# Kernel tuning notes

Hardware: AMD Instinct MI355X
Metric: run time of the kernel (lower is better)

## Reference

```python
import jax, jax.numpy as jnp
import numpy as np

N_XI = 512      # internal REN state dim
L = 128         # nonlinearity channels (sequential loop length)
N_STATES = 128  # plant state dim (w)
N_INPUTS = 64   # control input dim (u)
EPS = 0.001
STD = 0.1
BATCH = 32768


def _model_params(X, Y):
    """set_model_param(): derive constrained REN matrices from free params X, Y."""
    n, l = N_XI, L
    H = X.T @ X + EPS * jnp.eye(2 * n + l, dtype=X.dtype)
    H11 = H[:n, :n]
    H21 = H[n:n + l, :n]
    H22 = H[n:n + l, n:n + l]
    H31 = H[n + l:, :n]
    H32 = H[n + l:, n:n + l]
    H33 = H[n + l:, n + l:]
    Fm = H31                                 # (n_xi, n_xi)
    B1 = H32                                 # (n_xi, l)
    E = 0.5 * (H11 + H33 + Y - Y.T)          # (n_xi, n_xi)
    Lam = 0.5 * jnp.diag(H22)                # (l,) strictly positive
    D11 = -jnp.tril(H22, -1)                 # strictly lower triangular (l, l)
    C1 = -H21                                # (l, n_xi)
    return Fm, B1, E, Lam, D11, C1


def setup_inputs() -> dict:
    key = jax.random.key(0)
    ks = jax.random.split(key, 9)
    n, l = N_XI, L
    return {
        "t": 0,
        "w": jax.random.normal(ks[0], (BATCH, 1, N_STATES), jnp.float32),
        "xi": jax.random.normal(ks[1], (BATCH, 1, n), jnp.float32),
        "X": jax.random.normal(ks[2], (2 * n + l, 2 * n + l), jnp.float32) * STD,
        "Y": jax.random.normal(ks[3], (n, n), jnp.float32) * STD,
        "B2": jax.random.normal(ks[4], (n, N_STATES), jnp.float32) * STD,
        "C2": jax.random.normal(ks[5], (N_INPUTS, n), jnp.float32) * STD,
        "D21": jax.random.normal(ks[6], (N_INPUTS, l), jnp.float32) * STD,
        "D22": jax.random.normal(ks[7], (N_INPUTS, N_STATES), jnp.float32) * STD,
        "D12": jax.random.normal(ks[8], (l, N_STATES), jnp.float32) * STD,
    }


def reference(t, w, xi, X, Y, B2, C2, D21, D22, D12):
    Fm, B1, E, Lam, D11, C1 = _model_params(X, Y)
    w2 = w[:, 0, :]    # (B, num_states)
    xi2 = xi[:, 0, :]  # (B, n_xi)

    # Precompute the xi- and w-dependent parts of every row's pre-activation.
    pre = xi2 @ C1.T + w2 @ D12.T  # (B, l)

    eye = jnp.eye(L, dtype=pre.dtype)

    def step(eps, xs):
        # Sequential forward substitution: row i only reads eps[:, :i]
        # because D11 is strictly lower triangular.
        d_row, p_col, lam, e_row = xs
        v = p_col + eps @ d_row            # (B,)
        e = jnp.tanh(v / lam)
        return eps + e[:, None] * e_row[None, :], None

    eps0 = jnp.zeros_like(pre)
    epsilon, _ = jax.lax.scan(step, eps0, (D11, pre.T, Lam, eye))  # (B, l)

    E_xi = xi2 @ Fm.T + epsilon @ B1.T + w2 @ B2.T      # (B, n_xi)
    xi_ = E_xi @ jnp.linalg.inv(E).T                    # (B, n_xi)
    u = xi2 @ C2.T + epsilon @ D21.T + w2 @ D22.T       # (B, num_inputs)
    return u[:, None, :], xi_[:, None, :]
```

## Files before the change

### kernel.cpp

```cpp
#include <hip/hip_runtime.h>
#include <cstddef>

#define NXI   512
#define LL    128
#define NST   128
#define NU    64
#define BATCH 32768
#define TW    1152
#define EPSC  0.001f
#define KC    768
#define NC    576
#define NCP   640

typedef unsigned short u16;
typedef __attribute__((ext_vector_type(8))) short   short8;
typedef __attribute__((ext_vector_type(4))) short   short4v;
typedef __attribute__((ext_vector_type(4))) float   f32x4;

__device__ __forceinline__ u16 f2bf(float f) {
    unsigned u = __float_as_uint(f);
    u += 0x7FFFu + ((u >> 16) & 1u);
    return (u16)(u >> 16);
}

__global__ __launch_bounds__(256) void k_setup(const float* __restrict__ X, u16* __restrict__ XT,
                                               const float* __restrict__ xi, const float* __restrict__ w,
                                               u16* __restrict__ Ac) {
    __shared__ float t[32][33];
    int blk = blockIdx.x;
    if (blk < 1296) {
        int tx = threadIdx.x & 31, ty = threadIdx.x >> 5;
        int bx = blk % 36, by = blk / 36;
        #pragma unroll
        for (int q = 0; q < 4; q++) {
            int r = ty + q * 8;
            t[r][tx] = X[(size_t)(by * 32 + r) * TW + bx * 32 + tx];
        }
        __syncthreads();
        #pragma unroll
        for (int q = 0; q < 4; q++) {
            int r = ty + q * 8;
            XT[(size_t)(bx * 32 + r) * TW + by * 32 + tx] = f2bf(t[tx][r]);
        }
        return;
    }
    size_t tt = (size_t)(blk - 1296) * 256 + threadIdx.x;
    int b = (int)(tt / 80), ch = (int)(tt % 80);
    const float* src;
    int col;
    if (ch < 64) { src = xi + (size_t)b * NXI + ch * 8;        col = ch * 8; }
    else         { src = w  + (size_t)b * NST + (ch - 64) * 8; col = 640 + (ch - 64) * 8; }
    f32x4 a = ((const f32x4*)src)[0], c = ((const f32x4*)src)[1];
    short8 o;
    o[0]=(short)f2bf(a[0]); o[1]=(short)f2bf(a[1]); o[2]=(short)f2bf(a[2]); o[3]=(short)f2bf(a[3]);
    o[4]=(short)f2bf(c[0]); o[5]=(short)f2bf(c[1]); o[6]=(short)f2bf(c[2]); o[7]=(short)f2bf(c[3]);
    *(short8*)(Ac + (size_t)b * KC + col) = o;
}

__global__ __launch_bounds__(256) void k_gemm2(const u16* __restrict__ A, int lda,
                                               const u16* __restrict__ W, int ldw,
                                               float* __restrict__ C0, int ldc0, int nsplit,
                                               float* __restrict__ C1, int ldc1,
                                               int K, int nbx, int ntrue, int swz) {
    __shared__ __align__(16) u16 As[2][128 * 32];
    __shared__ __align__(16) u16 Bs[2][128 * 32];
    int id = blockIdx.x;
    int bx, by;
    if (swz) {
        int j = id >> 3;
        int per = (int)(gridDim.x >> 3) / nbx;
        by = (id & 7) * per + j / nbx;
        bx = j - (j / nbx) * nbx;
    } else {
        by = id / nbx;
        bx = id - by * nbx;
    }
    const int tid = threadIdx.x;
    const int wave = tid >> 6, lane = tid & 63, quad = lane >> 4, l16 = lane & 15;
    const int bm0 = by * 128, bn0 = bx * 128;
    const int srow = tid >> 2;
    const int sch = (((tid & 3) ^ ((srow >> 2) & 3))) * 8;
    const u16* ga0 = A + (size_t)(bm0 + srow) * lda + sch;
    const u16* ga1 = ga0 + (size_t)64 * lda;
    const u16* gb0 = W + (size_t)(bn0 + srow) * ldw + sch;
    const u16* gb1 = gb0 + (size_t)64 * ldw;
    const int lo = wave * 512;
    const int mb = (wave >> 1) * 64, nb = (wave & 1) * 64;
    const int rch = (quad ^ (l16 >> 2)) * 8;

    f32x4 acc[4][4];
    #pragma unroll
    for (int i = 0; i < 4; i++)
        #pragma unroll
        for (int j = 0; j < 4; j++) acc[i][j] = (f32x4){0.f, 0.f, 0.f, 0.f};

    const int nk = K >> 5;
    __builtin_amdgcn_global_load_lds((void*)(ga0), (void*)(As[0] + lo),        16, 0, 0);
    __builtin_amdgcn_global_load_lds((void*)(ga1), (void*)(As[0] + lo + 2048), 16, 0, 0);
    __builtin_amdgcn_global_load_lds((void*)(gb0), (void*)(Bs[0] + lo),        16, 0, 0);
    __builtin_amdgcn_global_load_lds((void*)(gb1), (void*)(Bs[0] + lo + 2048), 16, 0, 0);
    __syncthreads();
    int cur = 0;
    for (int t = 0; t < nk; ++t) {
        if (t + 1 < nk) {
            const int kt = (t + 1) << 5;
            const int nx = cur ^ 1;
            __builtin_amdgcn_global_load_lds((void*)(ga0 + kt), (void*)(As[nx] + lo),        16, 0, 0);
            __builtin_amdgcn_global_load_lds((void*)(ga1 + kt), (void*)(As[nx] + lo + 2048), 16, 0, 0);
            __builtin_amdgcn_global_load_lds((void*)(gb0 + kt), (void*)(Bs[nx] + lo),        16, 0, 0);
            __builtin_amdgcn_global_load_lds((void*)(gb1 + kt), (void*)(Bs[nx] + lo + 2048), 16, 0, 0);
        }
        const u16* as = As[cur];
        const u16* bs = Bs[cur];
        short8 af[4], bf[4];
        #pragma unroll
        for (int mt = 0; mt < 4; mt++) af[mt] = *(const short8*)&as[(mb + mt * 16 + l16) * 32 + rch];
        #pragma unroll
        for (int nt = 0; nt < 4; nt++) bf[nt] = *(const short8*)&bs[(nb + nt * 16 + l16) * 32 + rch];
        #pragma unroll
        for (int mt = 0; mt < 4; mt++)
            #pragma unroll
            for (int nt = 0; nt < 4; nt++)
                acc[mt][nt] = __builtin_amdgcn_mfma_f32_16x16x32_bf16(af[mt], bf[nt], acc[mt][nt], 0, 0, 0);
        __syncthreads();
        cur ^= 1;
    }
    #pragma unroll
    for (int mt = 0; mt < 4; mt++)
        #pragma unroll
        for (int nt = 0; nt < 4; nt++)
            #pragma unroll
            for (int r = 0; r < 4; r++) {
                int row = bm0 + mb + mt * 16 + quad * 4 + r;
                int col = bn0 + nb + nt * 16 + l16;
                if (col < ntrue) {
                    float v = acc[mt][nt][r];
                    if (col < nsplit) C0[(size_t)row * ldc0 + col] = v;
                    else              C1[(size_t)row * ldc1 + (col - nsplit)] = v;
                }
            }
}

__global__ __launch_bounds__(256) void k_derive(const float* __restrict__ Hm, const float* __restrict__ Y,
                                                const float* __restrict__ B2, const float* __restrict__ D12,
                                                float* __restrict__ Agj, float* __restrict__ D11,
                                                float* __restrict__ rlam, u16* __restrict__ W1) {
    int idx = blockIdx.x * 256 + threadIdx.x;
    const int n0 = 512 * 1280, n1 = 128 * 128, n2 = 128, n3 = 128 * KC;
    if (idx < n0) {
        int i = idx / 1280, j = idx % 1280;
        float val;
        if (j < 512) {
            val = 0.5f * (Hm[(size_t)i * TW + j] + Hm[(size_t)(640 + i) * TW + 640 + j]
                          + Y[(size_t)i * 512 + j] - Y[(size_t)j * 512 + i]);
            if (i == j) val += EPSC;
        } else if (j < 1024) {
            val = Hm[(size_t)(640 + i) * TW + (j - 512)];
        } else if (j < 1152) {
            val = Hm[(size_t)(640 + i) * TW + 512 + (j - 1024)];
        } else {
            val = B2[(size_t)i * NST + (j - 1152)];
        }
        Agj[idx] = val;
        return;
    }
    idx -= n0;
    if (idx < n1) {
        int i = idx >> 7, j = idx & 127;
        D11[idx] = (j < i) ? -Hm[(size_t)(512 + i) * TW + 512 + j] : 0.f;
        return;
    }
    idx -= n1;
    if (idx < n2) {
        rlam[idx] = 2.0f / (Hm[(size_t)(512 + idx) * TW + 512 + idx] + EPSC);
        return;
    }
    idx -= n2;
    if (idx < n3) {
        int i = idx / KC, c = idx % KC;
        float v;
        if (c < 512)      v = -Hm[(size_t)(512 + i) * TW + c];
        else if (c < 640) v = 0.f;
        else              v = D12[(size_t)i * NST + (c - 640)];
        W1[(size_t)i * KC + c] = f2bf(v);
    }
}

__device__ __forceinline__ void invert64ip(float* Cl, float* Sa, float* mcol, float* rp,
                                           float* __restrict__ invOut, int tid) {
    int r = tid >> 2, c = tid & 3;
    float a[16];
    #pragma unroll
    for (int q = 0; q < 4; q++) {
        f32x4 v = *(f32x4*)&Cl[r * 68 + c * 16 + q * 4];
        a[q*4+0]=v[0]; a[q*4+1]=v[1]; a[q*4+2]=v[2]; a[q*4+3]=v[3];
    }
    #pragma unroll
    for (int k = 0; k < 64; k++) {
        const int p = (k & 1) << 6;
        const int kc = k >> 4, kl = k & 15;
        if (r == k) {
            #pragma unroll
            for (int q = 0; q < 4; q++)
                *(f32x4*)&Sa[p + c * 16 + q * 4] = (f32x4){a[q*4], a[q*4+1], a[q*4+2], a[q*4+3]};
        }
        if (c == kc) {
            mcol[p + r] = a[kl];
            if (r == k) rp[k & 1] = 1.0f / a[kl];
        }
        __syncthreads();
        const bool piv = (r == k);
        float ip = rp[k & 1];
        float m  = mcol[p + r];
        float tm = piv ? ip : -m * ip;
        #pragma unroll
        for (int j = 0; j < 16; j++) {
            float sj = Sa[p + c * 16 + j];
            a[j] = fmaf(tm, sj, piv ? 0.f : a[j]);
        }
        if (c == kc) a[kl] = tm;
    }
    #pragma unroll
    for (int q = 0; q < 4; q++)
        *(f32x4*)&invOut[r * 64 + c * 16 + q * 4] = (f32x4){a[q*4], a[q*4+1], a[q*4+2], a[q*4+3]};
}

__global__ __launch_bounds__(256) void k_diaginv0(const float* __restrict__ Agj, float* __restrict__ invD,
                                                  const u16* __restrict__ Ac, const u16* __restrict__ W1,
                                                  float* __restrict__ pre) {
    __shared__ __align__(16) u16 AsB[2][4096];
    __shared__ __align__(16) u16 BsB[2][4096];
    __shared__ __align__(16) float Cl[64 * 68];
    __shared__ float Sa[128], mcol[128], rp[2];
    const int tid = threadIdx.x;
    const int id = blockIdx.x;
    if (id == 0) {
        int r = tid >> 2, c4 = tid & 3;
        #pragma unroll
        for (int q = 0; q < 4; q++)
            *(f32x4*)&Cl[r * 68 + c4 * 16 + q * 4] = *(const f32x4*)(Agj + (size_t)r * 1280 + c4 * 16 + q * 4);
        __syncthreads();
        invert64ip(Cl, Sa, mcol, rp, invD, tid);
        return;
    }
    const int by = id - 1;
    const int wave = tid >> 6, lane = tid & 63, quad = lane >> 4, l16 = lane & 15;
    const int bm0 = by * 128;
    const int srow = tid >> 2;
    const int sch = (((tid & 3) ^ ((srow >> 2) & 3))) * 8;
    const u16* ga0 = Ac + (size_t)(bm0 + srow) * KC + sch;
    const u16* ga1 = ga0 + (size_t)64 * KC;
    const u16* gb0 = W1 + (size_t)srow * KC + sch;
    const u16* gb1 = gb0 + (size_t)64 * KC;
    const int lo = wave * 512;
    const int mb = (wave >> 1) * 64, nb = (wave & 1) * 64;
    const int rch = (quad ^ (l16 >> 2)) * 8;
    f32x4 acc[4][4];
    #pragma unroll
    for (int i = 0; i < 4; i++)
        #pragma unroll
        for (int j = 0; j < 4; j++) acc[i][j] = (f32x4){0.f, 0.f, 0.f, 0.f};
    __builtin_amdgcn_global_load_lds((void*)(ga0), (void*)(AsB[0] + lo),        16, 0, 0);
    __builtin_amdgcn_global_load_lds((void*)(ga1), (void*)(AsB[0] + lo + 2048), 16, 0, 0);
    __builtin_amdgcn_global_load_lds((void*)(gb0), (void*)(BsB[0] + lo),        16, 0, 0);
    __builtin_amdgcn_global_load_lds((void*)(gb1), (void*)(BsB[0] + lo + 2048), 16, 0, 0);
    __syncthreads();
    int cur = 0;
    for (int t = 0; t < 24; ++t) {
        if (t + 1 < 24) {
            const int kt = (t + 1) << 5;
            const int nx = cur ^ 1;
            __builtin_amdgcn_global_load_lds((void*)(ga0 + kt), (void*)(AsB[nx] + lo),        16, 0, 0);
            __builtin_amdgcn_global_load_lds((void*)(ga1 + kt), (void*)(AsB[nx] + lo + 2048), 16, 0, 0);
            __builtin_amdgcn_global_load_lds((void*)(gb0 + kt), (void*)(BsB[nx] + lo),        16, 0, 0);
            __builtin_amdgcn_global_load_lds((void*)(gb1 + kt), (void*)(BsB[nx] + lo + 2048), 16, 0, 0);
        }
        const u16* as = AsB[cur];
        const u16* bs = BsB[cur];
        short8 af[4], bf[4];
        #pragma unroll
        for (int mt = 0; mt < 4; mt++) af[mt] = *(const short8*)&as[(mb + mt * 16 + l16) * 32 + rch];
        #pragma unroll
        for (int nt = 0; nt < 4; nt++) bf[nt] = *(const short8*)&bs[(nb + nt * 16 + l16) * 32 + rch];
        #pragma unroll
        for (int mt = 0; mt < 4; mt++)
            #pragma unroll
            for (int nt = 0; nt < 4; nt++)
                acc[mt][nt] = __builtin_amdgcn_mfma_f32_16x16x32_bf16(af[mt], bf[nt], acc[mt][nt], 0, 0, 0);
        __syncthreads();
        cur ^= 1;
    }
    #pragma unroll
    for (int mt = 0; mt < 4; mt++)
        #pragma unroll
        for (int nt = 0; nt < 4; nt++)
            #pragma unroll
            for (int r = 0; r < 4; r++)
                pre[(size_t)(bm0 + mb + mt * 16 + quad * 4 + r) * LL + (nb + nt * 16 + l16)] = acc[mt][nt][r];
}

__global__ __launch_bounds__(256) void k_elim(float* __restrict__ Agj, float* __restrict__ invD, int k) {
    __shared__ __align__(16) float invDs[64 * 68];
    __shared__ __align__(16) float Ps[64 * 68];
    __shared__ __align__(16) float Ss[64 * 68];
    __shared__ __align__(16) float Ms[64 * 68];
    __shared__ float Sa[128], mcol[128], rp[2];
    int tid = threadIdx.x;
    int by = blockIdx.y, bx = blockIdx.x;
    int rb = by + (by >= k ? 1 : 0);
    int cb = k + 1 + bx;
    int lr = tid >> 2, lc = tid & 3;
    #pragma unroll
    for (int q = 0; q < 4; q++) {
        *(f32x4*)&invDs[lr * 68 + lc * 16 + q * 4] = *(const f32x4*)(invD + (size_t)k * 4096 + lr * 64 + lc * 16 + q * 4);
        *(f32x4*)&Ps[lr * 68 + lc * 16 + q * 4]    = *(const f32x4*)(Agj + (size_t)(k * 64 + lr) * 1280 + cb * 64 + lc * 16 + q * 4);
        *(f32x4*)&Ms[lr * 68 + lc * 16 + q * 4]    = *(const f32x4*)(Agj + (size_t)(rb * 64 + lr) * 1280 + k * 64 + lc * 16 + q * 4);
    }
    __syncthreads();
    int ty = tid >> 4, tx = tid & 15;
    f32x4 s[4];
    #pragma unroll
    for (int ri = 0; ri < 4; ri++) s[ri] = (f32x4){0.f, 0.f, 0.f, 0.f};
    for (int kk = 0; kk < 64; kk++) {
        f32x4 pv = *(f32x4*)&Ps[kk * 68 + tx * 4];
        #pragma unroll
        for (int ri = 0; ri < 4; ri++) s[ri] += pv * invDs[(ty * 4 + ri) * 68 + kk];
    }
    #pragma unroll
    for (int ri = 0; ri < 4; ri++) *(f32x4*)&Ss[(ty * 4 + ri) * 68 + tx * 4] = s[ri];
    __syncthreads();
    f32x4 accv[4];
    #pragma unroll
    for (int ri = 0; ri < 4; ri++)
        accv[ri] = *(const f32x4*)(Agj + (size_t)(rb * 64 + ty * 4 + ri) * 1280 + cb * 64 + tx * 4);
    for (int kk = 0; kk < 64; kk++) {
        f32x4 sv = *(f32x4*)&Ss[kk * 68 + tx * 4];
        #pragma unroll
        for (int ri = 0; ri < 4; ri++) accv[ri] -= sv * Ms[(ty * 4 + ri) * 68 + kk];
    }
    #pragma unroll
    for (int ri = 0; ri < 4; ri++)
        *(f32x4*)(Agj + (size_t)(rb * 64 + ty * 4 + ri) * 1280 + cb * 64 + tx * 4) = accv[ri];
    if (k < 7 && bx == 0 && by == k) {
        __syncthreads();
        #pragma unroll
        for (int ri = 0; ri < 4; ri++) *(f32x4*)&Ps[(ty * 4 + ri) * 68 + tx * 4] = accv[ri];
        __syncthreads();
        invert64ip(Ps, Sa, mcol, rp, invD + (size_t)(k + 1) * 4096, tid);
    }
}

__global__ __launch_bounds__(256) void k_finalize(const float* __restrict__ Agj, const float* __restrict__ invD,
                                                  const float* __restrict__ C2, const float* __restrict__ D21,
                                                  const float* __restrict__ D22, u16* __restrict__ Wc) {
    __shared__ __align__(16) float invDs[64 * 68];
    __shared__ __align__(16) float Ps[64 * 68];
    int tid = threadIdx.x, bx = blockIdx.x, by = blockIdx.y;
    int ty = tid >> 4, tx = tid & 15;
    if (by >= 8) {
        #pragma unroll
        for (int ri = 0; ri < 4; ri++) {
            int q = ty * 4 + ri;
            int row = 512 + (by - 8) * 64 + q;
            int cbase = bx * 64 + tx * 4;
            short4v o;
            if (by == 8) {
                f32x4 v;
                if (cbase < 512)      v = *(const f32x4*)(C2 + (size_t)q * 512 + cbase);
                else if (cbase < 640) v = *(const f32x4*)(D21 + (size_t)q * NST + (cbase - 512));
                else                  v = *(const f32x4*)(D22 + (size_t)q * NST + (cbase - 640));
                o[0]=(short)f2bf(v[0]); o[1]=(short)f2bf(v[1]); o[2]=(short)f2bf(v[2]); o[3]=(short)f2bf(v[3]);
            } else {
                o[0]=0; o[1]=0; o[2]=0; o[3]=0;
            }
            *(short4v*)(Wc + (size_t)row * KC + cbase) = o;
        }
        return;
    }
    int lr = tid >> 2, lc = tid & 3;
    #pragma unroll
    for (int q = 0; q < 4; q++) {
        *(f32x4*)&invDs[lr * 68 + lc * 16 + q * 4] = *(const f32x4*)(invD + (size_t)by * 4096 + lr * 64 + lc * 16 + q * 4);
        *(f32x4*)&Ps[lr * 68 + lc * 16 + q * 4]    = *(const f32x4*)(Agj + (size_t)(by * 64 + lr) * 1280 + 512 + bx * 64 + lc * 16 + q * 4);
    }
    __syncthreads();
    f32x4 s[4];
    #pragma unroll
    for (int ri = 0; ri < 4; ri++) s[ri] = (f32x4){0.f, 0.f, 0.f, 0.f};
    for (int kk = 0; kk < 64; kk++) {
        f32x4 pv = *(f32x4*)&Ps[kk * 68 + tx * 4];
        #pragma unroll
        for (int ri = 0; ri < 4; ri++) s[ri] += pv * invDs[(ty * 4 + ri) * 68 + kk];
    }
    #pragma unroll
    for (int ri = 0; ri < 4; ri++) {
        short4v o; o[0]=(short)f2bf(s[ri][0]); o[1]=(short)f2bf(s[ri][1]); o[2]=(short)f2bf(s[ri][2]); o[3]=(short)f2bf(s[ri][3]);
        *(short4v*)(Wc + (size_t)(by * 64 + ty * 4 + ri) * KC + bx * 64 + tx * 4) = o;
    }
}

__global__ __launch_bounds__(1024) void k_scan(const float* __restrict__ pre, const float* __restrict__ D11,
                                               const float* __restrict__ rlam, u16* __restrict__ Ac) {
    __shared__ __align__(16) float D11s[128 * 132];
    int tid = threadIdx.x;
    {
        int r = tid >> 3, c = (tid & 7) * 16;
        const f32x4* src = (const f32x4*)(D11 + (size_t)r * 128 + c);
        f32x4 v0 = src[0], v1 = src[1], v2 = src[2], v3 = src[3];
        f32x4* dst = (f32x4*)&D11s[r * 132 + c];
        dst[0] = v0; dst[1] = v1; dst[2] = v2; dst[3] = v3;
    }
    int lg = tid & 15;
    int row = blockIdx.x * 64 + (tid >> 4);
    int gbase = (tid & 63) & ~15;
    const float L2E2 = 2.885390082f;

    float corrv[8], a8[8];
    #pragma unroll
    for (int b = 0; b < 8; b++) {
        corrv[b] = pre[(size_t)row * 128 + b * 16 + lg];
        a8[b] = L2E2 * rlam[b * 16 + lg];
    }
    __syncthreads();

    #pragma unroll
    for (int b = 0; b < 8; b++) {
        f32x4 dblk[4];
        #pragma unroll
        for (int q = 0; q < 4; q++)
            dblk[q] = *(const f32x4*)&D11s[(b * 16 + lg) * 132 + b * 16 + q * 4];
        float v = corrv[b];
        float a = a8[b];
        float e16[16];
        float myeps = 0.f;
        #pragma unroll
        for (int t = 0; t < 16; t++) {
            float ex = __builtin_amdgcn_exp2f(a * v);
            float cand = 1.0f - 2.0f * __builtin_amdgcn_rcpf(ex + 1.0f);
            float e = __shfl(cand, gbase + t, 64);
            e16[t] = e;
            if (lg == t) myeps = e;
            v = fmaf(e, dblk[t >> 2][t & 3], v);
        }
        Ac[(size_t)row * KC + 512 + b * 16 + lg] = f2bf(myeps);
        #pragma unroll
        for (int bb = b + 1; bb < 8; bb++) {
            f32x4 dd[4];
            #pragma unroll
            for (int q = 0; q < 4; q++)
                dd[q] = *(const f32x4*)&D11s[(bb * 16 + lg) * 132 + b * 16 + q * 4];
            float acc = corrv[bb];
            #pragma unroll
            for (int t = 0; t < 16; t++)
                acc = fmaf(e16[t], dd[t >> 2][t & 3], acc);
            corrv[bb] = acc;
        }
    }
}

extern "C" void kernel_launch(void* const* d_in, const int* in_sizes, int n_in,
                              void* d_out, int out_size, void* d_ws, size_t ws_size,
                              hipStream_t stream) {
    const float* w_in  = (const float*)d_in[1];
    const float* xi_in = (const float*)d_in[2];
    const float* X   = (const float*)d_in[3];
    const float* Y   = (const float*)d_in[4];
    const float* B2  = (const float*)d_in[5];
    const float* C2  = (const float*)d_in[6];
    const float* D21 = (const float*)d_in[7];
    const float* D22 = (const float*)d_in[8];
    const float* D12 = (const float*)d_in[9];
    float* out_u  = (float*)d_out;
    float* out_xi = (float*)d_out + (size_t)BATCH * NU;

    char* base = (char*)d_ws;
    size_t off = 0;
    auto carve = [&](size_t bytes) -> void* {
        void* p = base + off;
        off += (bytes + 255) & ~(size_t)255;
        return p;
    };
    u16*   XT   = (u16*)  carve((size_t)TW * TW * 2);
    u16*   Ac   = (u16*)  carve((size_t)BATCH * KC * 2);
    float* Hm   = (float*)carve((size_t)TW * TW * 4);
    float* Agj  = (float*)carve((size_t)512 * 1280 * 4);
    float* invD = (float*)carve((size_t)8 * 64 * 64 * 4);
    u16*   Wc   = (u16*)  carve((size_t)NCP * KC * 2);
    u16*   W1   = (u16*)  carve((size_t)LL * KC * 2);
    float* pre  = (float*)carve((size_t)BATCH * LL * 4);
    float* D11  = (float*)carve((size_t)LL * LL * 4);
    float* rlam = (float*)carve((size_t)LL * 4);
    (void)ws_size; (void)in_sizes; (void)n_in; (void)out_size;

    k_setup<<<1296 + BATCH * 80 / 256, 256, 0, stream>>>(X, XT, xi_in, w_in, Ac);
    k_gemm2<<<81, 256, 0, stream>>>(XT, TW, XT, TW, Hm, TW, 1 << 30, nullptr, 0, TW, 9, TW, 0);
    k_derive<<<(512 * 1280 + 128 * 128 + 128 + 128 * KC + 255) / 256, 256, 0, stream>>>(
        Hm, Y, B2, D12, Agj, D11, rlam, W1);
    k_diaginv0<<<257, 256, 0, stream>>>(Agj, invD, Ac, W1, pre);
    for (int k = 0; k < 8; k++)
        k_elim<<<dim3(19 - k, 7), 256, 0, stream>>>(Agj, invD, k);
    k_finalize<<<dim3(12, 10), 256, 0, stream>>>(Agj, invD, C2, D21, D22, Wc);
    k_scan<<<BATCH / 64, 1024, 0, stream>>>(pre, D11, rlam, Ac);
    k_gemm2<<<1280, 256, 0, stream>>>(Ac, KC, Wc, KC, out_xi, NXI, 512, out_u, NU, KC, 5, NC, 1);
}
```

Measured before the change: 479.4 us.

## Fuse block Gauss-Jordan elimination steps and finalize into one persistent kernel

```diff
diff --git a/kernel.cpp b/kernel.cpp
--- a/kernel.cpp
+++ b/kernel.cpp
@@ -11,6 +11,7 @@
 #define KC    768
 #define NC    576
 #define NCP   640
+#define GJB   133
 
 typedef unsigned short u16;
 typedef __attribute__((ext_vector_type(8))) short   short8;
@@ -21,6 +22,36 @@
     unsigned u = __float_as_uint(f);
     u += 0x7FFFu + ((u >> 16) & 1u);
     return (u16)(u >> 16);
+}
+
+__device__ __forceinline__ void fbar(int* flags, int* go, int nblk, int tv, int id) {
+    __syncthreads();
+    const int t = threadIdx.x;
+    if (id == 0) {
+        if (t >= 1 && t < nblk) {
+            int spins = 0;
+            while (__hip_atomic_load(flags + t, __ATOMIC_RELAXED, __HIP_MEMORY_SCOPE_AGENT) < tv) {
+                __builtin_amdgcn_s_sleep(2);
+                if (++spins > (1 << 18)) break;
+            }
+        }
+        __syncthreads();
+        if (t == 0) {
+            __threadfence();
+            __hip_atomic_store(go, tv, __ATOMIC_RELEASE, __HIP_MEMORY_SCOPE_AGENT);
+        }
+    } else {
+        if (t == 0) {
+            __hip_atomic_store(flags + id, tv, __ATOMIC_RELEASE, __HIP_MEMORY_SCOPE_AGENT);
+            int spins = 0;
+            while (__hip_atomic_load(go, __ATOMIC_RELAXED, __HIP_MEMORY_SCOPE_AGENT) < tv) {
+                __builtin_amdgcn_s_sleep(2);
+                if (++spins > (1 << 18)) break;
+            }
+            __threadfence();
+        }
+    }
+    __syncthreads();
 }
 
 __global__ __launch_bounds__(256) void k_setup(const float* __restrict__ X, u16* __restrict__ XT,
@@ -144,7 +175,9 @@
 __global__ __launch_bounds__(256) void k_derive(const float* __restrict__ Hm, const float* __restrict__ Y,
                                                 const float* __restrict__ B2, const float* __restrict__ D12,
                                                 float* __restrict__ Agj, float* __restrict__ D11,
-                                                float* __restrict__ rlam, u16* __restrict__ W1) {
+                                                float* __restrict__ rlam, u16* __restrict__ W1,
+                                                int* __restrict__ bar) {
+    if (blockIdx.x == 0 && threadIdx.x < 192) bar[threadIdx.x] = 0;
     int idx = blockIdx.x * 256 + threadIdx.x;
     const int n0 = 512 * 1280, n1 = 128 * 128, n2 = 128, n3 = 128 * KC;
     if (idx < n0) {
@@ -299,103 +332,114 @@
                 pre[(size_t)(bm0 + mb + mt * 16 + quad * 4 + r) * LL + (nb + nt * 16 + l16)] = acc[mt][nt][r];
 }
 
-__global__ __launch_bounds__(256) void k_elim(float* __restrict__ Agj, float* __restrict__ invD, int k) {
+__global__ __launch_bounds__(256) void k_gj_fused(
+        float* __restrict__ Agj, float* __restrict__ invD,
+        const float* __restrict__ C2, const float* __restrict__ D21,
+        const float* __restrict__ D22, u16* __restrict__ Wc,
+        int* __restrict__ bar) {
     __shared__ __align__(16) float invDs[64 * 68];
     __shared__ __align__(16) float Ps[64 * 68];
     __shared__ __align__(16) float Ss[64 * 68];
     __shared__ __align__(16) float Ms[64 * 68];
     __shared__ float Sa[128], mcol[128], rp[2];
-    int tid = threadIdx.x;
-    int by = blockIdx.y, bx = blockIdx.x;
-    int rb = by + (by >= k ? 1 : 0);
-    int cb = k + 1 + bx;
-    int lr = tid >> 2, lc = tid & 3;
-    #pragma unroll
-    for (int q = 0; q < 4; q++) {
-        *(f32x4*)&invDs[lr * 68 + lc * 16 + q * 4] = *(const f32x4*)(invD + (size_t)k * 4096 + lr * 64 + lc * 16 + q * 4);
-        *(f32x4*)&Ps[lr * 68 + lc * 16 + q * 4]    = *(const f32x4*)(Agj + (size_t)(k * 64 + lr) * 1280 + cb * 64 + lc * 16 + q * 4);
-        *(f32x4*)&Ms[lr * 68 + lc * 16 + q * 4]    = *(const f32x4*)(Agj + (size_t)(rb * 64 + lr) * 1280 + k * 64 + lc * 16 + q * 4);
-    }
-    __syncthreads();
-    int ty = tid >> 4, tx = tid & 15;
-    f32x4 s[4];
-    #pragma unroll
-    for (int ri = 0; ri < 4; ri++) s[ri] = (f32x4){0.f, 0.f, 0.f, 0.f};
-    for (int kk = 0; kk < 64; kk++) {
-        f32x4 pv = *(f32x4*)&Ps[kk * 68 + tx * 4];
-        #pragma unroll
-        for (int ri = 0; ri < 4; ri++) s[ri] += pv * invDs[(ty * 4 + ri) * 68 + kk];
-    }
-    #pragma unroll
-    for (int ri = 0; ri < 4; ri++) *(f32x4*)&Ss[(ty * 4 + ri) * 68 + tx * 4] = s[ri];
-    __syncthreads();
-    f32x4 accv[4];
-    #pragma unroll
-    for (int ri = 0; ri < 4; ri++)
-        accv[ri] = *(const f32x4*)(Agj + (size_t)(rb * 64 + ty * 4 + ri) * 1280 + cb * 64 + tx * 4);
-    for (int kk = 0; kk < 64; kk++) {
-        f32x4 sv = *(f32x4*)&Ss[kk * 68 + tx * 4];
-        #pragma unroll
-        for (int ri = 0; ri < 4; ri++) accv[ri] -= sv * Ms[(ty * 4 + ri) * 68 + kk];
-    }
-    #pragma unroll
-    for (int ri = 0; ri < 4; ri++)
-        *(f32x4*)(Agj + (size_t)(rb * 64 + ty * 4 + ri) * 1280 + cb * 64 + tx * 4) = accv[ri];
-    if (k < 7 && bx == 0 && by == k) {
-        __syncthreads();
-        #pragma unroll
-        for (int ri = 0; ri < 4; ri++) *(f32x4*)&Ps[(ty * 4 + ri) * 68 + tx * 4] = accv[ri];
-        __syncthreads();
-        invert64ip(Ps, Sa, mcol, rp, invD + (size_t)(k + 1) * 4096, tid);
-    }
-}
-
-__global__ __launch_bounds__(256) void k_finalize(const float* __restrict__ Agj, const float* __restrict__ invD,
-                                                  const float* __restrict__ C2, const float* __restrict__ D21,
-                                                  const float* __restrict__ D22, u16* __restrict__ Wc) {
-    __shared__ __align__(16) float invDs[64 * 68];
-    __shared__ __align__(16) float Ps[64 * 68];
-    int tid = threadIdx.x, bx = blockIdx.x, by = blockIdx.y;
-    int ty = tid >> 4, tx = tid & 15;
-    if (by >= 8) {
+    const int tid = threadIdx.x;
+    const int id = blockIdx.x;
+    int* flags = bar;
+    int* go    = bar + 160;
+
+    for (int k = 0; k < 8; ++k) {
+        const int nbk = 7 * (19 - k);
+        if (id < nbk) {
+            const int by = id % 7, bx = id / 7;
+            const int rb = by + (by >= k ? 1 : 0);
+            const int cb = k + 1 + bx;
+            int lr = tid >> 2, lc = tid & 3;
+            #pragma unroll
+            for (int q = 0; q < 4; q++) {
+                *(f32x4*)&invDs[lr * 68 + lc * 16 + q * 4] = *(const f32x4*)(invD + (size_t)k * 4096 + lr * 64 + lc * 16 + q * 4);
+                *(f32x4*)&Ps[lr * 68 + lc * 16 + q * 4]    = *(const f32x4*)(Agj + (size_t)(k * 64 + lr) * 1280 + cb * 64 + lc * 16 + q * 4);
+                *(f32x4*)&Ms[lr * 68 + lc * 16 + q * 4]    = *(const f32x4*)(Agj + (size_t)(rb * 64 + lr) * 1280 + k * 64 + lc * 16 + q * 4);
+            }
+            __syncthreads();
+            int ty = tid >> 4, tx = tid & 15;
+            f32x4 s[4];
+            #pragma unroll
+            for (int ri = 0; ri < 4; ri++) s[ri] = (f32x4){0.f, 0.f, 0.f, 0.f};
+            for (int kk = 0; kk < 64; kk++) {
+                f32x4 pv = *(f32x4*)&Ps[kk * 68 + tx * 4];
+                #pragma unroll
+                for (int ri = 0; ri < 4; ri++) s[ri] += pv * invDs[(ty * 4 + ri) * 68 + kk];
+            }
+            #pragma unroll
+            for (int ri = 0; ri < 4; ri++) *(f32x4*)&Ss[(ty * 4 + ri) * 68 + tx * 4] = s[ri];
+            __syncthreads();
+            f32x4 accv[4];
+            #pragma unroll
+            for (int ri = 0; ri < 4; ri++)
+                accv[ri] = *(const f32x4*)(Agj + (size_t)(rb * 64 + ty * 4 + ri) * 1280 + cb * 64 + tx * 4);
+            for (int kk = 0; kk < 64; kk++) {
+                f32x4 sv = *(f32x4*)&Ss[kk * 68 + tx * 4];
+                #pragma unroll
+                for (int ri = 0; ri < 4; ri++) accv[ri] -= sv * Ms[(ty * 4 + ri) * 68 + kk];
+            }
+            #pragma unroll
+            for (int ri = 0; ri < 4; ri++)
+                *(f32x4*)(Agj + (size_t)(rb * 64 + ty * 4 + ri) * 1280 + cb * 64 + tx * 4) = accv[ri];
+            if (k < 7 && bx == 0 && by == k) {
+                __syncthreads();
+                #pragma unroll
+                for (int ri = 0; ri < 4; ri++) *(f32x4*)&Ps[(ty * 4 + ri) * 68 + tx * 4] = accv[ri];
+                __syncthreads();
+                invert64ip(Ps, Sa, mcol, rp, invD + (size_t)(k + 1) * 4096, tid);
+            }
+        }
+        fbar(flags, go, GJB, k + 1, id);
+    }
+
+    if (id < 120) {
+        const int bx = id % 12, by = id / 12;
+        int ty = tid >> 4, tx = tid & 15;
+        if (by >= 8) {
+            #pragma unroll
+            for (int ri = 0; ri < 4; ri++) {
+                int q = ty * 4 + ri;
+                int row = 512 + (by - 8) * 64 + q;
+                int cbase = bx * 64 + tx * 4;
+                short4v o;
+                if (by == 8) {
+                    f32x4 v;
+                    if (cbase < 512)      v = *(const f32x4*)(C2 + (size_t)q * 512 + cbase);
+                    else if (cbase < 640) v = *(const f32x4*)(D21 + (size_t)q * NST + (cbase - 512));
+                    else                  v = *(const f32x4*)(D22 + (size_t)q * NST + (cbase - 640));
+                    o[0]=(short)f2bf(v[0]); o[1]=(short)f2bf(v[1]); o[2]=(short)f2bf(v[2]); o[3]=(short)f2bf(v[3]);
+                } else {
+                    o[0]=0; o[1]=0; o[2]=0; o[3]=0;
+                }
+                *(short4v*)(Wc + (size_t)row * KC + cbase) = o;
+            }
+            return;
+        }
+        int lr = tid >> 2, lc = tid & 3;
+        #pragma unroll
+        for (int q = 0; q < 4; q++) {
+            *(f32x4*)&invDs[lr * 68 + lc * 16 + q * 4] = *(const f32x4*)(invD + (size_t)by * 4096 + lr * 64 + lc * 16 + q * 4);
+            *(f32x4*)&Ps[lr * 68 + lc * 16 + q * 4]    = *(const f32x4*)(Agj + (size_t)(by * 64 + lr) * 1280 + 512 + bx * 64 + lc * 16 + q * 4);
+        }
+        __syncthreads();
+        int ty2 = tid >> 4, tx2 = tid & 15;
+        f32x4 s[4];
+        #pragma unroll
+        for (int ri = 0; ri < 4; ri++) s[ri] = (f32x4){0.f, 0.f, 0.f, 0.f};
+        for (int kk = 0; kk < 64; kk++) {
+            f32x4 pv = *(f32x4*)&Ps[kk * 68 + tx2 * 4];
+            #pragma unroll
+            for (int ri = 0; ri < 4; ri++) s[ri] += pv * invDs[(ty2 * 4 + ri) * 68 + kk];
+        }
         #pragma unroll
         for (int ri = 0; ri < 4; ri++) {
-            int q = ty * 4 + ri;
-            int row = 512 + (by - 8) * 64 + q;
-            int cbase = bx * 64 + tx * 4;
-            short4v o;
-            if (by == 8) {
-                f32x4 v;
-                if (cbase < 512)      v = *(const f32x4*)(C2 + (size_t)q * 512 + cbase);
-                else if (cbase < 640) v = *(const f32x4*)(D21 + (size_t)q * NST + (cbase - 512));
-                else                  v = *(const f32x4*)(D22 + (size_t)q * NST + (cbase - 640));
-                o[0]=(short)f2bf(v[0]); o[1]=(short)f2bf(v[1]); o[2]=(short)f2bf(v[2]); o[3]=(short)f2bf(v[3]);
-            } else {
-                o[0]=0; o[1]=0; o[2]=0; o[3]=0;
-            }
-            *(short4v*)(Wc + (size_t)row * KC + cbase) = o;
-        }
-        return;
-    }
-    int lr = tid >> 2, lc = tid & 3;
-    #pragma unroll
-    for (int q = 0; q < 4; q++) {
-        *(f32x4*)&invDs[lr * 68 + lc * 16 + q * 4] = *(const f32x4*)(invD + (size_t)by * 4096 + lr * 64 + lc * 16 + q * 4);
-        *(f32x4*)&Ps[lr * 68 + lc * 16 + q * 4]    = *(const f32x4*)(Agj + (size_t)(by * 64 + lr) * 1280 + 512 + bx * 64 + lc * 16 + q * 4);
-    }
-    __syncthreads();
-    f32x4 s[4];
-    #pragma unroll
-    for (int ri = 0; ri < 4; ri++) s[ri] = (f32x4){0.f, 0.f, 0.f, 0.f};
-    for (int kk = 0; kk < 64; kk++) {
-        f32x4 pv = *(f32x4*)&Ps[kk * 68 + tx * 4];
-        #pragma unroll
-        for (int ri = 0; ri < 4; ri++) s[ri] += pv * invDs[(ty * 4 + ri) * 68 + kk];
-    }
-    #pragma unroll
-    for (int ri = 0; ri < 4; ri++) {
-        short4v o; o[0]=(short)f2bf(s[ri][0]); o[1]=(short)f2bf(s[ri][1]); o[2]=(short)f2bf(s[ri][2]); o[3]=(short)f2bf(s[ri][3]);
-        *(short4v*)(Wc + (size_t)(by * 64 + ty * 4 + ri) * KC + bx * 64 + tx * 4) = o;
+            short4v o; o[0]=(short)f2bf(s[ri][0]); o[1]=(short)f2bf(s[ri][1]); o[2]=(short)f2bf(s[ri][2]); o[3]=(short)f2bf(s[ri][3]);
+            *(short4v*)(Wc + (size_t)(by * 64 + ty2 * 4 + ri) * KC + bx * 64 + tx2 * 4) = o;
+        }
     }
 }
 
@@ -490,16 +534,15 @@
     float* pre  = (float*)carve((size_t)BATCH * LL * 4);
     float* D11  = (float*)carve((size_t)LL * LL * 4);
     float* rlam = (float*)carve((size_t)LL * 4);
+    int*   bar  = (int*)  carve(1024);
     (void)ws_size; (void)in_sizes; (void)n_in; (void)out_size;
 
     k_setup<<<1296 + BATCH * 80 / 256, 256, 0, stream>>>(X, XT, xi_in, w_in, Ac);
     k_gemm2<<<81, 256, 0, stream>>>(XT, TW, XT, TW, Hm, TW, 1 << 30, nullptr, 0, TW, 9, TW, 0);
     k_derive<<<(512 * 1280 + 128 * 128 + 128 + 128 * KC + 255) / 256, 256, 0, stream>>>(
-        Hm, Y, B2, D12, Agj, D11, rlam, W1);
+        Hm, Y, B2, D12, Agj, D11, rlam, W1, bar);
     k_diaginv0<<<257, 256, 0, stream>>>(Agj, invD, Ac, W1, pre);
-    for (int k = 0; k < 8; k++)
-        k_elim<<<dim3(19 - k, 7), 256, 0, stream>>>(Agj, invD, k);
-    k_finalize<<<dim3(12, 10), 256, 0, stream>>>(Agj, invD, C2, D21, D22, Wc);
+    k_gj_fused<<<GJB, 256, 0, stream>>>(Agj, invD, C2, D21, D22, Wc, bar);
     k_scan<<<BATCH / 64, 1024, 0, stream>>>(pre, D11, rlam, Ac);
     k_gemm2<<<1280, 256, 0, stream>>>(Ac, KC, Wc, KC, out_xi, NXI, 512, out_u, NU, KC, 5, NC, 1);
 }
```

Result: slower. 525.9 us (+9.7%).
